# Performance work log

Hardware: AMD Instinct MI355X
Metric: run time of the kernel (lower is better)

## Reference

```python
import jax, jax.numpy as jnp
import numpy as np

IN_DIM = 128
HIDDEN = 128


def setup_inputs() -> dict:
    key = jax.random.key(0)
    k1, k2, k3, k4, k5 = jax.random.split(key, 5)
    bound_ih = 1.0 / np.sqrt(IN_DIM)
    bound_hh = 1.0 / np.sqrt(HIDDEN)
    return {
        "x": jax.random.normal(k1, (256, 2048, IN_DIM), dtype=jnp.float32),
        "W_ih": jax.random.uniform(k2, (HIDDEN, IN_DIM), minval=-bound_ih, maxval=bound_ih, dtype=jnp.float32),
        "b_ih": jax.random.uniform(k3, (HIDDEN,), minval=-bound_ih, maxval=bound_ih, dtype=jnp.float32),
        "W_hh": jax.random.uniform(k4, (HIDDEN, HIDDEN), minval=-bound_hh, maxval=bound_hh, dtype=jnp.float32),
        "b_hh": jax.random.uniform(k5, (HIDDEN,), minval=-bound_hh, maxval=bound_hh, dtype=jnp.float32),
    }


def reference(x, W_ih, b_ih, W_hh, b_hh):
    B, S, _ = x.shape
    # Precompute input projection for all timesteps in one big GEMM: [B,S,H]
    xw = jnp.einsum("bsi,hi->bsh", x, W_ih) + b_ih
    h0 = jnp.zeros((B, W_hh.shape[0]), dtype=x.dtype)

    def step(h, xw_t):
        h_new = jnp.tanh(xw_t + h @ W_hh.T + b_hh)
        return h_new, None

    # scan over time axis: move S to leading dim
    h_final, _ = jax.lax.scan(step, h0, jnp.swapaxes(xw, 0, 1))
    return h_final
```

## Files before the change

### kernel.cpp

```cpp
#include <hip/hip_runtime.h>


#define BATCH 256
#define SEQ   2048
#define HID   128
#define CH    16
#define NCHUNK (SEQ / CH)

template <int CTRL>
__device__ __forceinline__ float dpp_movf(float x) {
    return __int_as_float(__builtin_amdgcn_mov_dpp(__float_as_int(x), CTRL, 0xF, 0xF, true));
}

__device__ __forceinline__ float tanh_fast(float x) {
    x = fminf(fmaxf(x, -12.0f), 12.0f);
    float e = __expf(2.0f * x);
    return 1.0f - __fdividef(2.0f, e + 1.0f);
}

__global__ __launch_bounds__(512, 2) void rnn_scan_kernel(
    const float* __restrict__ x,
    const float* __restrict__ Wih,
    const float* __restrict__ bih,
    const float* __restrict__ Whh,
    const float* __restrict__ bhh,
    float* __restrict__ out)
{
    const int b = blockIdx.x;
    const int t = threadIdx.x;
    const int g = t >> 4;
    const int c = t & 15;
    const int colbase = c << 3;
    const int rowbase = g << 2;

    __shared__ __align__(16) float xbuf[2][CH * HID];
    __shared__ __align__(16) float hbuf[2][192];

    float4 wi[4][2], wh[4][2];
#pragma unroll
    for (int r = 0; r < 4; ++r) {
        const float* pi = Wih + (rowbase + r) * HID + colbase;
        const float* ph = Whh + (rowbase + r) * HID + colbase;
        wi[r][0] = *(const float4*)(pi);
        wi[r][1] = *(const float4*)(pi + 4);
        wh[r][0] = *(const float4*)(ph);
        wh[r][1] = *(const float4*)(ph + 4);
    }

    const int m = c & 3;
    const int o = ((m & 1) << 1) | ((m >> 1) & 1);
    const int row0 = rowbase + o;
    const float bias = bih[row0] + bhh[row0];
    const int hw = row0 + ((row0 >> 3) << 2);

    const int bx = (c >> 2) & 1;
    const int xoff0 = (((c << 1) ^ bx) << 2);
    const int xoff1 = ((((c << 1) | 1) ^ bx) << 2);
    const int sidx = t ^ ((t >> 3) & 1);

    const float* xsrc = x + (size_t)b * (SEQ * HID);

    {
        const float4* gp = (const float4*)xsrc;
        ((float4*)&xbuf[0][0])[sidx] = gp[t];
    }
    if (t < 192) hbuf[0][t] = 0.0f;
    __syncthreads();

    int cur = 0;
    for (int chn = 0; chn < NCHUNK; ++chn) {
        float4 q0;
        const bool pf = (chn + 1 < NCHUNK);
        if (pf) {
            const float4* gp = (const float4*)(xsrc + (size_t)(chn + 1) * (CH * HID));
            q0 = gp[t];
        }
        const float* xb = &xbuf[chn & 1][0];
#pragma unroll 1
        for (int s = 0; s < CH; ++s) {
            const float* xr = xb + s * HID;
            const float* hr = &hbuf[cur][12 * c];
            float4 hv0 = *(const float4*)(hr);
            float4 hv1 = *(const float4*)(hr + 4);
            float4 xv0 = *(const float4*)(xr + xoff0);
            float4 xv1 = *(const float4*)(xr + xoff1);

            float a[4];
#pragma unroll
            for (int r = 0; r < 4; ++r) {
                float acc;
                acc = wi[r][0].x * xv0.x;
                acc = fmaf(wi[r][0].y, xv0.y, acc);
                acc = fmaf(wi[r][0].z, xv0.z, acc);
                acc = fmaf(wi[r][0].w, xv0.w, acc);
                acc = fmaf(wi[r][1].x, xv1.x, acc);
                acc = fmaf(wi[r][1].y, xv1.y, acc);
                acc = fmaf(wi[r][1].z, xv1.z, acc);
                acc = fmaf(wi[r][1].w, xv1.w, acc);
                acc = fmaf(wh[r][0].x, hv0.x, acc);
                acc = fmaf(wh[r][0].y, hv0.y, acc);
                acc = fmaf(wh[r][0].z, hv0.z, acc);
                acc = fmaf(wh[r][0].w, hv0.w, acc);
                acc = fmaf(wh[r][1].x, hv1.x, acc);
                acc = fmaf(wh[r][1].y, hv1.y, acc);
                acc = fmaf(wh[r][1].z, hv1.z, acc);
                acc = fmaf(wh[r][1].w, hv1.w, acc);
                a[r] = acc;
            }

            const bool b0 = (c & 1) != 0;
            const bool b1 = (c & 2) != 0;
            float k0 = b0 ? a[2] : a[0], s0 = b0 ? a[0] : a[2];
            float k1 = b0 ? a[3] : a[1], s1 = b0 ? a[1] : a[3];
            float t0 = k0 + dpp_movf<0xB1>(s0);
            float t1 = k1 + dpp_movf<0xB1>(s1);
            float k2 = b1 ? t1 : t0, s2 = b1 ? t0 : t1;
            float u = k2 + dpp_movf<0x4E>(s2);
            u += dpp_movf<0x124>(u);
            u += dpp_movf<0x128>(u);

            float h = tanh_fast(u + bias);
            if (c < 4) {
                hbuf[cur ^ 1][hw] = h;
            }

            if (s == CH - 1 && pf) {
                ((float4*)&xbuf[(chn + 1) & 1][0])[sidx] = q0;
            }
            __syncthreads();
            cur ^= 1;
        }
    }
    if (t < HID) out[(size_t)b * HID + t] = hbuf[cur][t + ((t >> 3) << 2)];
}

extern "C" void kernel_launch(void* const* d_in, const int* in_sizes, int n_in,
                              void* d_out, int out_size, void* d_ws, size_t ws_size,
                              hipStream_t stream) {
    const float* x   = (const float*)d_in[0];
    const float* Wih = (const float*)d_in[1];
    const float* bih = (const float*)d_in[2];
    const float* Whh = (const float*)d_in[3];
    const float* bhh = (const float*)d_in[4];
    float* out = (float*)d_out;

    rnn_scan_kernel<<<BATCH, 512, 0, stream>>>(x, Wih, bih, Whh, bhh, out);
}
```

Before: 1.106 ms.

## Compute input projection per chunk with split-bf16 MFMA, off the recurrent path

Moves the x·W_ih projection out of the per-step scalar FMA chain. Each 16-step chunk is now computed up front with bf16 MFMA instructions, using a hi/lo split (three products) to keep near-fp32 accuracy. The results are staged in shared memory, and the serial step only adds one precomputed value per row. The pipeline is extended to convert x two chunks ahead into a swizzled bf16 layout. The cost is more shared memory and a burst of MFMA work at step 0 of each chunk, with some accuracy risk from the bf16 split approximation.

```diff
diff --git a/kernel.cpp b/kernel.cpp
--- a/kernel.cpp
+++ b/kernel.cpp
@@ -7,6 +7,9 @@
 #define CH    16
 #define NCHUNK (SEQ / CH)
 
+typedef __attribute__((ext_vector_type(8))) short bf16x8;
+typedef __attribute__((ext_vector_type(4))) float f32x4;
+
 template <int CTRL>
 __device__ __forceinline__ float dpp_movf(float x) {
     return __int_as_float(__builtin_amdgcn_mov_dpp(__float_as_int(x), CTRL, 0xF, 0xF, true));
@@ -16,6 +19,16 @@
     x = fminf(fmaxf(x, -12.0f), 12.0f);
     float e = __expf(2.0f * x);
     return 1.0f - __fdividef(2.0f, e + 1.0f);
+}
+
+__device__ __forceinline__ void bf16_split(float v, short& hi, short& lo) {
+    unsigned u = __float_as_uint(v);
+    unsigned hb = (u + 0x8000u) & 0xFFFF0000u;
+    float hf = __uint_as_float(hb);
+    float r = v - hf;
+    unsigned ru = __float_as_uint(r);
+    hi = (short)(hb >> 16);
+    lo = (short)((ru + 0x8000u) >> 16);
 }
 
 __global__ __launch_bounds__(512, 2) void rnn_scan_kernel(
@@ -32,19 +45,38 @@
     const int c = t & 15;
     const int colbase = c << 3;
     const int rowbase = g << 2;
-
-    __shared__ __align__(16) float xbuf[2][CH * HID];
-    __shared__ __align__(16) float hbuf[2][192];
-
-    float4 wi[4][2], wh[4][2];
+    const int lane = t & 63;
+    const int w = t >> 6;
+
+    __shared__ __align__(16) ushort xbf[2][2][CH * HID];
+    __shared__ __align__(16) float  xwbuf[2][CH * HID];
+    __shared__ __align__(16) float  hbuf[2][192];
+
+    float4 wh[4][2];
 #pragma unroll
     for (int r = 0; r < 4; ++r) {
-        const float* pi = Wih + (rowbase + r) * HID + colbase;
         const float* ph = Whh + (rowbase + r) * HID + colbase;
-        wi[r][0] = *(const float4*)(pi);
-        wi[r][1] = *(const float4*)(pi + 4);
         wh[r][0] = *(const float4*)(ph);
         wh[r][1] = *(const float4*)(ph + 4);
+    }
+
+    const int bcol = (w << 4) + (lane & 15);
+    const int krow = (lane >> 4) << 3;
+    bf16x8 bhi[4], blo[4];
+#pragma unroll
+    for (int kk = 0; kk < 4; ++kk) {
+        const float* src = Wih + bcol * HID + kk * 32 + krow;
+        float4 u0 = *(const float4*)(src);
+        float4 u1 = *(const float4*)(src + 4);
+        short hh, ll;
+        bf16_split(u0.x, hh, ll); bhi[kk][0] = hh; blo[kk][0] = ll;
+        bf16_split(u0.y, hh, ll); bhi[kk][1] = hh; blo[kk][1] = ll;
+        bf16_split(u0.z, hh, ll); bhi[kk][2] = hh; blo[kk][2] = ll;
+        bf16_split(u0.w, hh, ll); bhi[kk][3] = hh; blo[kk][3] = ll;
+        bf16_split(u1.x, hh, ll); bhi[kk][4] = hh; blo[kk][4] = ll;
+        bf16_split(u1.y, hh, ll); bhi[kk][5] = hh; blo[kk][5] = ll;
+        bf16_split(u1.z, hh, ll); bhi[kk][6] = hh; blo[kk][6] = ll;
+        bf16_split(u1.w, hh, ll); bhi[kk][7] = hh; blo[kk][7] = ll;
     }
 
     const int m = c & 3;
@@ -53,51 +85,82 @@
     const float bias = bih[row0] + bhh[row0];
     const int hw = row0 + ((row0 >> 3) << 2);
 
-    const int bx = (c >> 2) & 1;
-    const int xoff0 = (((c << 1) ^ bx) << 2);
-    const int xoff1 = ((((c << 1) | 1) ^ bx) << 2);
-    const int sidx = t ^ ((t >> 3) & 1);
-
     const float* xsrc = x + (size_t)b * (SEQ * HID);
+
+    auto stage_bf16 = [&](float4 q, int buf) {
+        const int srow = t >> 5;
+        const int sw = ((srow << 8) + ((t & 31) << 3)) ^ ((srow & 7) << 4);
+        short h0, l0, h1, l1, h2, l2, h3, l3;
+        bf16_split(q.x, h0, l0); bf16_split(q.y, h1, l1);
+        bf16_split(q.z, h2, l2); bf16_split(q.w, h3, l3);
+        uint2 ph, pl;
+        ph.x = (unsigned)(ushort)h0 | ((unsigned)(ushort)h1 << 16);
+        ph.y = (unsigned)(ushort)h2 | ((unsigned)(ushort)h3 << 16);
+        pl.x = (unsigned)(ushort)l0 | ((unsigned)(ushort)l1 << 16);
+        pl.y = (unsigned)(ushort)l2 | ((unsigned)(ushort)l3 << 16);
+        *(uint2*)((char*)&xbf[buf][0][0] + sw) = ph;
+        *(uint2*)((char*)&xbf[buf][1][0] + sw) = pl;
+    };
+
+    auto compute_xw = [&](int mm) {
+        const int buf = mm & 1;
+        const int arow = lane & 15;
+        const int rowb = (arow << 8) + ((lane >> 4) << 4);
+        const int swz = (arow & 7) << 4;
+        const char* hp = (const char*)&xbf[buf][0][0];
+        const char* lp = (const char*)&xbf[buf][1][0];
+        f32x4 acc0 = {0.0f, 0.0f, 0.0f, 0.0f};
+        f32x4 acc1 = {0.0f, 0.0f, 0.0f, 0.0f};
+#pragma unroll
+        for (int kk = 0; kk < 4; ++kk) {
+            const int off = (rowb + kk * 64) ^ swz;
+            bf16x8 ah = *(const bf16x8*)(hp + off);
+            bf16x8 al = *(const bf16x8*)(lp + off);
+            f32x4& acc = (kk & 1) ? acc1 : acc0;
+            acc = __builtin_amdgcn_mfma_f32_16x16x32_bf16(ah, bhi[kk], acc, 0, 0, 0);
+            acc = __builtin_amdgcn_mfma_f32_16x16x32_bf16(ah, blo[kk], acc, 0, 0, 0);
+            acc = __builtin_amdgcn_mfma_f32_16x16x32_bf16(al, bhi[kk], acc, 0, 0, 0);
+        }
+        float* xw = &xwbuf[buf][0];
+        const int crow = (lane >> 4) << 2;
+#pragma unroll
+        for (int r = 0; r < 4; ++r) xw[(crow + r) * HID + bcol] = acc0[r] + acc1[r];
+    };
 
     {
         const float4* gp = (const float4*)xsrc;
-        ((float4*)&xbuf[0][0])[sidx] = gp[t];
+        float4 a0 = gp[t];
+        float4 a1 = gp[512 + t];
+        stage_bf16(a0, 0);
+        stage_bf16(a1, 1);
     }
     if (t < 192) hbuf[0][t] = 0.0f;
     __syncthreads();
+    compute_xw(0);
+    __syncthreads();
 
     int cur = 0;
-    for (int chn = 0; chn < NCHUNK; ++chn) {
+    for (int n = 0; n < NCHUNK; ++n) {
         float4 q0;
-        const bool pf = (chn + 1 < NCHUNK);
+        const bool pf = (n + 2 < NCHUNK);
         if (pf) {
-            const float4* gp = (const float4*)(xsrc + (size_t)(chn + 1) * (CH * HID));
+            const float4* gp = (const float4*)(xsrc + (size_t)(n + 2) * (CH * HID));
             q0 = gp[t];
         }
-        const float* xb = &xbuf[chn & 1][0];
+        const float* xwc = &xwbuf[n & 1][0];
 #pragma unroll 1
         for (int s = 0; s < CH; ++s) {
-            const float* xr = xb + s * HID;
+            float xwv = 0.0f;
+            if (c < 4) xwv = xwc[s * HID + row0];
             const float* hr = &hbuf[cur][12 * c];
             float4 hv0 = *(const float4*)(hr);
             float4 hv1 = *(const float4*)(hr + 4);
-            float4 xv0 = *(const float4*)(xr + xoff0);
-            float4 xv1 = *(const float4*)(xr + xoff1);
 
             float a[4];
 #pragma unroll
             for (int r = 0; r < 4; ++r) {
                 float acc;
-                acc = wi[r][0].x * xv0.x;
-                acc = fmaf(wi[r][0].y, xv0.y, acc);
-                acc = fmaf(wi[r][0].z, xv0.z, acc);
-                acc = fmaf(wi[r][0].w, xv0.w, acc);
-                acc = fmaf(wi[r][1].x, xv1.x, acc);
-                acc = fmaf(wi[r][1].y, xv1.y, acc);
-                acc = fmaf(wi[r][1].z, xv1.z, acc);
-                acc = fmaf(wi[r][1].w, xv1.w, acc);
-                acc = fmaf(wh[r][0].x, hv0.x, acc);
+                acc = wh[r][0].x * hv0.x;
                 acc = fmaf(wh[r][0].y, hv0.y, acc);
                 acc = fmaf(wh[r][0].z, hv0.z, acc);
                 acc = fmaf(wh[r][0].w, hv0.w, acc);
@@ -119,14 +182,14 @@
             u += dpp_movf<0x124>(u);
             u += dpp_movf<0x128>(u);
 
-            float h = tanh_fast(u + bias);
+            float hval = tanh_fast(u + bias + xwv);
             if (c < 4) {
-                hbuf[cur ^ 1][hw] = h;
+                hbuf[cur ^ 1][hw] = hval;
             }
 
-            if (s == CH - 1 && pf) {
-                ((float4*)&xbuf[(chn + 1) & 1][0])[sidx] = q0;
-            }
+            if (s == 0 && n + 1 < NCHUNK) compute_xw(n + 1);
+            if (s == CH - 1 && pf) stage_bf16(q0, n & 1);
+
             __syncthreads();
             cur ^= 1;
         }
```

Measured after the change: 1.082 ms. 1.02x faster.
